# Kernel optimization log

Measured on AMD Instinct MI355X. Metric: run time of the kernel, lower is better.

Reference implementation:

```python
import jax, jax.numpy as jnp
import numpy as np

B, S, H, NH = 32, 512, 2048, 8
HD = H // NH
MAXPOS = 1000


def _sinusoidal_pe():
    pos = np.arange(MAXPOS)[:, None].astype(np.float32)
    div = np.exp(np.arange(0, H, 2).astype(np.float32) * (-np.log(10000.0) / H))
    pe = np.zeros((1, MAXPOS, H), np.float32)
    pe[0, :, 0::2] = np.sin(pos * div)
    pe[0, :, 1::2] = np.cos(pos * div)
    return jnp.asarray(pe)


def setup_inputs() -> dict:
    key = jax.random.key(0)
    ks = jax.random.split(key, 12)
    w = lambda k, shape: jax.random.normal(k, shape, jnp.float32) * 0.02
    return {
        'embeddings': jax.random.normal(ks[0], (B, S, H), jnp.float32),
        'temporal_indices': jax.random.randint(ks[1], (B, S), 0, MAXPOS),
        'pe': _sinusoidal_pe(),
        'in_proj_w': w(ks[2], (3 * H, H)), 'in_proj_b': jnp.zeros((3 * H,), jnp.float32),
        'out_proj_w': w(ks[3], (H, H)), 'out_proj_b': jnp.zeros((H,), jnp.float32),
        'ln1_g': jnp.ones((H,), jnp.float32), 'ln1_b': jnp.zeros((H,), jnp.float32),
        'ffn_w1': w(ks[4], (4 * H, H)), 'ffn_b1': jnp.zeros((4 * H,), jnp.float32),
        'ffn_w2': w(ks[5], (H, 4 * H)), 'ffn_b2': jnp.zeros((H,), jnp.float32),
        'ln2_g': jnp.ones((H,), jnp.float32), 'ln2_b': jnp.zeros((H,), jnp.float32),
        'te_w1': w(ks[6], (H, H)), 'te_b1': jnp.zeros((H,), jnp.float32),
        'te_w2': w(ks[7], (H, H)), 'te_b2': jnp.zeros((H,), jnp.float32),
        'pr_w1': w(ks[8], (H, H)), 'pr_b1': jnp.zeros((H,), jnp.float32),
        'pr_w2': w(ks[9], (H, H)), 'pr_b2': jnp.zeros((H,), jnp.float32),
    }


def _ln(x, g, b, eps=1e-5):
    m = jnp.mean(x, -1, keepdims=True)
    v = jnp.mean((x - m) ** 2, -1, keepdims=True)
    return (x - m) * jax.lax.rsqrt(v + eps) * g + b


def _forward(embeddings, pe, in_proj_w, in_proj_b, out_proj_w, out_proj_b,
             ln1_g, ln1_b, ffn_w1, ffn_b1, ffn_w2, ffn_b2, ln2_g, ln2_b,
             te_w1, te_b1, te_w2, te_b2, pr_w1, pr_b1, pr_w2, pr_b2,
             temporal_indices):
    b, s, h = embeddings.shape
    # temporal positional encoding gather: [B,S,H]
    x = embeddings + pe[0][temporal_indices]
    # packed qkv projection (torch MultiheadAttention in_proj)
    qkv = x @ in_proj_w.T + in_proj_b
    q, k, v = jnp.split(qkv, 3, axis=-1)
    heads = lambda t: t.reshape(b, s, NH, HD).transpose(0, 2, 1, 3)
    q, k, v = heads(q), heads(k), heads(v)
    scores = jnp.einsum('bhqd,bhkd->bhqk', q, k) / jnp.sqrt(jnp.float32(HD))
    a = jax.nn.softmax(scores, axis=-1)
    o = jnp.einsum('bhqk,bhkd->bhqd', a, v).transpose(0, 2, 1, 3).reshape(b, s, h)
    attn = o @ out_proj_w.T + out_proj_b
    # residual + LN, GELU FFN, residual + LN
    h1 = _ln(embeddings + attn, ln1_g, ln1_b)
    f = jax.nn.gelu(h1 @ ffn_w1.T + ffn_b1, approximate=False) @ ffn_w2.T + ffn_b2
    h2 = _ln(h1 + f, ln2_g, ln2_b)
    # temporal_encoder MLP (temporal_info=None branch)
    te = jax.nn.relu(h2 @ te_w1.T + te_b1) @ te_w2.T + te_b2
    # projection head (training-mode path)
    pr = jax.nn.relu(te @ pr_w1.T + pr_b1) @ pr_w2.T + pr_b2
    return pr / jnp.maximum(jnp.linalg.norm(pr, axis=-1, keepdims=True), 1e-12)


def reference(embeddings, temporal_indices, pe, in_proj_w, in_proj_b, out_proj_w,
              out_proj_b, ln1_g, ln1_b, ffn_w1, ffn_b1, ffn_w2, ffn_b2, ln2_g,
              ln2_b, te_w1, te_b1, te_w2, te_b2, pr_w1, pr_b1, pr_w2, pr_b2):
    return _forward(embeddings, pe, in_proj_w, in_proj_b, out_proj_w, out_proj_b,
                    ln1_g, ln1_b, ffn_w1, ffn_b1, ffn_w2, ffn_b2, ln2_g, ln2_b,
                    te_w1, te_b1, te_w2, te_b2, pr_w1, pr_b1, pr_w2, pr_b2,
                    temporal_indices)
```

## Files before the change

### kernel.cpp

```cpp
#include <hip/hip_runtime.h>
#include <math.h>


typedef __bf16 bf16;
typedef __bf16 bf16x8 __attribute__((ext_vector_type(8)));
typedef float f32x4 __attribute__((ext_vector_type(4)));

#define Hdim 2048

#define GLOAD_LDS16(gp, lp)                                          \
  __builtin_amdgcn_global_load_lds(                                  \
      (const __attribute__((address_space(1))) void*)(gp),           \
      (__attribute__((address_space(3))) void*)(lp), 16, 0, 0)

template <int RF>
__global__ __launch_bounds__(256)
void gemm_bt(const bf16* __restrict__ A, int lda, long sA1, long sA2, int zdA,
             const bf16* __restrict__ W, int ldw, long sW1, long sW2, int zdW,
             bf16* __restrict__ C, int ldc, long sC1, long sC2, int zdC,
             const float* __restrict__ bias,
             const void* __restrict__ resp, int ldr,
             int K, float scale, int act)
{
  __shared__ bf16 As[2][128 * 64];
  __shared__ bf16 Ws[2][128 * 64];
  const int tid = threadIdx.x;
  const int z = blockIdx.z;
  A += (size_t)(z / zdA) * sA1 + (size_t)(z % zdA) * sA2;
  W += (size_t)(z / zdW) * sW1 + (size_t)(z % zdW) * sW2;
  C += (size_t)(z / zdC) * sC1 + (size_t)(z % zdC) * sC2;

  const int nwg = gridDim.x * gridDim.y;
  int bid = blockIdx.y * gridDim.x + blockIdx.x;
  bid = (bid & 7) * (nwg >> 3) + (bid >> 3);
  const int m0 = (bid / gridDim.x) * 128, n0 = (bid % gridDim.x) * 128;

  const int sm = tid >> 3;
  const int swz = ((tid & 7) ^ (sm & 7)) * 8;
  const int lane = tid & 63, quad = lane >> 4, lr = lane & 15;
  const int wid = tid >> 6, wm = wid >> 1, wn = wid & 1;
  const int rx = lr & 7;
  const int so0 = ((quad      ) ^ rx) * 8;
  const int so1 = ((quad | 4) ^ rx) * 8;

  f32x4 acc[4][4] = {};

  const bf16* Ag = A + (size_t)(m0 + sm) * lda + swz;
  const bf16* Wg = W + (size_t)(n0 + sm) * ldw + swz;

  const int nt = K >> 6;
#pragma unroll
  for (int s = 0; s < 4; ++s) {
    GLOAD_LDS16(Ag + (size_t)(s * 32) * lda, &As[0][s * 2048 + tid * 8]);
    GLOAD_LDS16(Wg + (size_t)(s * 32) * ldw, &Ws[0][s * 2048 + tid * 8]);
  }
  __syncthreads();

  for (int t = 0; t < nt; ++t) {
    const int cur = t & 1;
    if (t + 1 < nt) {
      const int k0 = (t + 1) << 6;
#pragma unroll
      for (int s = 0; s < 4; ++s) {
        GLOAD_LDS16(Ag + (size_t)(s * 32) * lda + k0, &As[cur ^ 1][s * 2048 + tid * 8]);
        GLOAD_LDS16(Wg + (size_t)(s * 32) * ldw + k0, &Ws[cur ^ 1][s * 2048 + tid * 8]);
      }
    }
    const bf16* Ab = As[cur];
    const bf16* Wb = Ws[cur];
#pragma unroll
    for (int kk = 0; kk < 2; ++kk) {
      const int so = kk ? so1 : so0;
      bf16x8 af[4], bfr[4];
#pragma unroll
      for (int i = 0; i < 4; ++i)
        af[i] = *(const bf16x8*)&Ab[(wm * 64 + i * 16 + lr) * 64 + so];
#pragma unroll
      for (int j = 0; j < 4; ++j)
        bfr[j] = *(const bf16x8*)&Wb[(wn * 64 + j * 16 + lr) * 64 + so];
#pragma unroll
      for (int i = 0; i < 4; ++i)
#pragma unroll
        for (int j = 0; j < 4; ++j)
          acc[i][j] = __builtin_amdgcn_mfma_f32_16x16x32_bf16(af[i], bfr[j], acc[i][j], 0, 0, 0);
    }
    __syncthreads();
  }

  float bj[4];
#pragma unroll
  for (int j = 0; j < 4; ++j)
    bj[j] = bias ? bias[n0 + wn * 64 + j * 16 + lr] : 0.0f;

#pragma unroll
  for (int i = 0; i < 4; ++i) {
#pragma unroll
    for (int r = 0; r < 4; ++r) {
      const int m = m0 + wm * 64 + i * 16 + quad * 4 + r;
#pragma unroll
      for (int j = 0; j < 4; ++j) {
        const int n = n0 + wn * 64 + j * 16 + lr;
        float v = acc[i][j][r] * scale + bj[j];
        if (resp) {
          if (RF) v += ((const float*)resp)[(size_t)m * ldr + n];
          else    v += (float)((const bf16*)resp)[(size_t)m * ldr + n];
        }
        if (act == 1) v = fmaxf(v, 0.0f);
        else if (act == 2) v = 0.5f * v * (1.0f + erff(v * 0.70710678118654752f));
        C[(size_t)m * ldc + n] = (bf16)v;
      }
    }
  }
}

__global__ __launch_bounds__(256)
void cvt_w(const float* __restrict__ src, bf16* __restrict__ dst)
{
  const size_t i = ((size_t)blockIdx.x * 256 + threadIdx.x) * 8;
  float4 a = *(const float4*)&src[i];
  float4 b = *(const float4*)&src[i + 4];
  bf16x8 o;
  o[0] = (bf16)a.x; o[1] = (bf16)a.y; o[2] = (bf16)a.z; o[3] = (bf16)a.w;
  o[4] = (bf16)b.x; o[5] = (bf16)b.y; o[6] = (bf16)b.z; o[7] = (bf16)b.w;
  *(bf16x8*)&dst[i] = o;
}

__global__ __launch_bounds__(256)
void gather_pe(const float* __restrict__ emb, const int* __restrict__ idx,
               const float* __restrict__ pe, bf16* __restrict__ X)
{
  const int m = blockIdx.x;
  const int p = idx[m];
  const size_t off = (size_t)m * Hdim + threadIdx.x * 8;
  const size_t poff = (size_t)p * Hdim + threadIdx.x * 8;
  float4 e0 = *(const float4*)&emb[off];
  float4 e1 = *(const float4*)&emb[off + 4];
  float4 q0 = *(const float4*)&pe[poff];
  float4 q1 = *(const float4*)&pe[poff + 4];
  bf16x8 o;
  o[0] = (bf16)(e0.x + q0.x); o[1] = (bf16)(e0.y + q0.y);
  o[2] = (bf16)(e0.z + q0.z); o[3] = (bf16)(e0.w + q0.w);
  o[4] = (bf16)(e1.x + q1.x); o[5] = (bf16)(e1.y + q1.y);
  o[6] = (bf16)(e1.z + q1.z); o[7] = (bf16)(e1.w + q1.w);
  *(bf16x8*)&X[off] = o;
}

__global__ __launch_bounds__(256)
void softmax_rows(bf16* __restrict__ P)
{
  const int lane = threadIdx.x & 63;
  const size_t row = (size_t)blockIdx.x * 4 + (threadIdx.x >> 6);
  bf16* p = P + row * 512 + lane * 8;
  bf16x8 v = *(const bf16x8*)p;
  float x[8], mx = -1e30f;
#pragma unroll
  for (int j = 0; j < 8; ++j) { x[j] = (float)v[j]; mx = fmaxf(mx, x[j]); }
#pragma unroll
  for (int o = 32; o; o >>= 1) mx = fmaxf(mx, __shfl_xor(mx, o));
  float s = 0.0f;
#pragma unroll
  for (int j = 0; j < 8; ++j) { x[j] = expf(x[j] - mx); s += x[j]; }
#pragma unroll
  for (int o = 32; o; o >>= 1) s += __shfl_xor(s, o);
  const float inv = 1.0f / s;
  bf16x8 ov;
#pragma unroll
  for (int j = 0; j < 8; ++j) ov[j] = (bf16)(x[j] * inv);
  *(bf16x8*)p = ov;
}

__global__ __launch_bounds__(256)
void transpose_v(const bf16* __restrict__ qkv, bf16* __restrict__ vt)
{
  const int z = blockIdx.z, b = z >> 3, h = z & 7;
  const unsigned short* V =
      (const unsigned short*)qkv + (size_t)b * 512 * 6144 + 4096 + h * 256;
  unsigned short* out = (unsigned short*)vt + (size_t)z * 256 * 512;
  const int d0 = blockIdx.x * 64, k0 = blockIdx.y * 64;
  __shared__ unsigned short t[64 * 65];
  const int r = threadIdx.x >> 3;
  const int c8 = (threadIdx.x & 7) * 8;
#pragma unroll
  for (int pass = 0; pass < 2; ++pass) {
    const int rr = r + pass * 32;
    uint4 u = *(const uint4*)(V + (size_t)(k0 + rr) * 6144 + d0 + c8);
    const unsigned short* ep = (const unsigned short*)&u;
#pragma unroll
    for (int j = 0; j < 8; ++j) t[(c8 + j) * 65 + rr] = ep[j];
  }
  __syncthreads();
#pragma unroll
  for (int pass = 0; pass < 2; ++pass) {
    const int dr = r + pass * 32;
    unsigned short e[8];
#pragma unroll
    for (int j = 0; j < 8; ++j) e[j] = t[dr * 65 + c8 + j];
    *(uint4*)(out + (size_t)(d0 + dr) * 512 + k0 + c8) = *(const uint4*)e;
  }
}

__global__ __launch_bounds__(256)
void ln_rows(const bf16* __restrict__ src, const float* __restrict__ g,
             const float* __restrict__ b, bf16* __restrict__ dst)
{
  const size_t off = (size_t)blockIdx.x * Hdim + threadIdx.x * 8;
  bf16x8 v = *(const bf16x8*)&src[off];
  float x[8], s = 0.0f, ss = 0.0f;
#pragma unroll
  for (int j = 0; j < 8; ++j) { x[j] = (float)v[j]; s += x[j]; ss += x[j] * x[j]; }
  __shared__ float red[8];
#pragma unroll
  for (int o = 32; o; o >>= 1) { s += __shfl_xor(s, o); ss += __shfl_xor(ss, o); }
  const int w = threadIdx.x >> 6;
  if ((threadIdx.x & 63) == 0) { red[w] = s; red[4 + w] = ss; }
  __syncthreads();
  s = red[0] + red[1] + red[2] + red[3];
  ss = red[4] + red[5] + red[6] + red[7];
  const float mean = s * (1.0f / Hdim);
  const float var = ss * (1.0f / Hdim) - mean * mean;
  const float rstd = rsqrtf(var + 1e-5f);
  float4 g0 = *(const float4*)&g[threadIdx.x * 8];
  float4 g1 = *(const float4*)&g[threadIdx.x * 8 + 4];
  float4 b0 = *(const float4*)&b[threadIdx.x * 8];
  float4 b1 = *(const float4*)&b[threadIdx.x * 8 + 4];
  const float gg[8] = {g0.x, g0.y, g0.z, g0.w, g1.x, g1.y, g1.z, g1.w};
  const float bb[8] = {b0.x, b0.y, b0.z, b0.w, b1.x, b1.y, b1.z, b1.w};
  bf16x8 ov;
#pragma unroll
  for (int j = 0; j < 8; ++j)
    ov[j] = (bf16)(((x[j] - mean) * rstd) * gg[j] + bb[j]);
  *(bf16x8*)&dst[off] = ov;
}

__global__ __launch_bounds__(256)
void l2norm_rows(const bf16* __restrict__ src, float* __restrict__ dst)
{
  const size_t off = (size_t)blockIdx.x * Hdim + threadIdx.x * 8;
  bf16x8 v = *(const bf16x8*)&src[off];
  float x[8], ss = 0.0f;
#pragma unroll
  for (int j = 0; j < 8; ++j) { x[j] = (float)v[j]; ss += x[j] * x[j]; }
  __shared__ float red[4];
#pragma unroll
  for (int o = 32; o; o >>= 1) ss += __shfl_xor(ss, o);
  const int w = threadIdx.x >> 6;
  if ((threadIdx.x & 63) == 0) red[w] = ss;
  __syncthreads();
  ss = red[0] + red[1] + red[2] + red[3];
  const float inv = 1.0f / fmaxf(sqrtf(ss), 1e-12f);
  float4 o0, o1;
  o0.x = x[0] * inv; o0.y = x[1] * inv; o0.z = x[2] * inv; o0.w = x[3] * inv;
  o1.x = x[4] * inv; o1.y = x[5] * inv; o1.z = x[6] * inv; o1.w = x[7] * inv;
  *(float4*)&dst[off] = o0;
  *(float4*)&dst[off + 4] = o1;
}

extern "C" void kernel_launch(void* const* d_in, const int* in_sizes, int n_in,
                              void* d_out, int out_size, void* d_ws, size_t ws_size,
                              hipStream_t stream)
{
  const float* emb  = (const float*)d_in[0];
  const int*   tix  = (const int*)d_in[1];
  const float* pe   = (const float*)d_in[2];
  const float* Wqkv = (const float*)d_in[3];
  const float* Bqkv = (const float*)d_in[4];
  const float* Wout = (const float*)d_in[5];
  const float* Bout = (const float*)d_in[6];
  const float* ln1g = (const float*)d_in[7];
  const float* ln1b = (const float*)d_in[8];
  const float* Wff1 = (const float*)d_in[9];
  const float* Bff1 = (const float*)d_in[10];
  const float* Wff2 = (const float*)d_in[11];
  const float* Bff2 = (const float*)d_in[12];
  const float* ln2g = (const float*)d_in[13];
  const float* ln2b = (const float*)d_in[14];
  const float* Wte1 = (const float*)d_in[15];
  const float* Bte1 = (const float*)d_in[16];
  const float* Wte2 = (const float*)d_in[17];
  const float* Bte2 = (const float*)d_in[18];
  const float* Wpr1 = (const float*)d_in[19];
  const float* Bpr1 = (const float*)d_in[20];
  const float* Wpr2 = (const float*)d_in[21];
  const float* Bpr2 = (const float*)d_in[22];
  float* OUT = (float*)d_out;

  char* w = (char*)d_ws;
  bf16* RA   = (bf16*)(w);
  bf16* RB   = (bf16*)(w + (64u << 20));
  bf16* QKVc = RB;
  char* ob   = (char*)d_out;
  bf16* Pc   = (bf16*)(ob);
  bf16* VTc  = (bf16*)(ob + (32u << 20));
  bf16* R1   = (bf16*)(ob);
  bf16* F1c  = (bf16*)(ob);
  bf16* WqkvB = (bf16*)(ob + (48u << 20));
  bf16* WoutB = (bf16*)(ob + (72u << 20));
  bf16* Wff1B = (bf16*)(ob + (64u << 20));
  bf16* Wff2B = (bf16*)(ob + (96u << 20));
  bf16* WteB1 = (bf16*)(ob);
  bf16* WteB2 = (bf16*)(ob + (8u << 20));
  bf16* WprB1 = (bf16*)(ob + (16u << 20));
  bf16* WprB2 = (bf16*)(ob + (24u << 20));

  cvt_w<<<6144, 256, 0, stream>>>(Wqkv, WqkvB);
  cvt_w<<<2048, 256, 0, stream>>>(Wout, WoutB);

  gather_pe<<<16384, 256, 0, stream>>>(emb, tix, pe, RA);

  for (int c = 0; c < 4; ++c) {
    const bf16* Xc = RA + (size_t)c * 4096 * 2048;
    bf16* Oc = RA + (size_t)c * 4096 * 2048;

    gemm_bt<0><<<dim3(48, 32, 1), 256, 0, stream>>>(
        Xc, 2048, 0, 0, 1, WqkvB, 2048, 0, 0, 1, QKVc, 6144, 0, 0, 1,
        Bqkv, nullptr, 0, 2048, 1.0f, 0);

    gemm_bt<0><<<dim3(4, 4, 64), 256, 0, stream>>>(
        QKVc, 6144, 3145728L, 256, 8,
        QKVc + 2048, 6144, 3145728L, 256, 8,
        Pc, 512, 262144L, 0, 1,
        nullptr, nullptr, 0, 256, 0.0625f, 0);

    softmax_rows<<<8192, 256, 0, stream>>>(Pc);

    transpose_v<<<dim3(4, 8, 64), 256, 0, stream>>>(QKVc, VTc);

    gemm_bt<0><<<dim3(2, 4, 64), 256, 0, stream>>>(
        Pc, 512, 262144L, 0, 1,
        VTc, 512, 131072L, 0, 1,
        Oc, 2048, 1048576L, 256, 8,
        nullptr, nullptr, 0, 512, 1.0f, 0);
  }

  gemm_bt<1><<<dim3(16, 128, 1), 256, 0, stream>>>(
      RA, 2048, 0, 0, 1, WoutB, 2048, 0, 0, 1, R1, 2048, 0, 0, 1,
      Bout, emb, 2048, 2048, 1.0f, 0);

  cvt_w<<<8192, 256, 0, stream>>>(Wff1, Wff1B);
  cvt_w<<<8192, 256, 0, stream>>>(Wff2, Wff2B);

  ln_rows<<<16384, 256, 0, stream>>>(R1, ln1g, ln1b, RA);

  for (int f = 0; f < 8; ++f) {
    const bf16* H1f = RA + (size_t)f * 2048 * 2048;
    bf16* R2f = RB + (size_t)f * 2048 * 2048;
    gemm_bt<0><<<dim3(64, 16, 1), 256, 0, stream>>>(
        H1f, 2048, 0, 0, 1, Wff1B, 2048, 0, 0, 1, F1c, 8192, 0, 0, 1,
        Bff1, nullptr, 0, 2048, 1.0f, 2);
    gemm_bt<0><<<dim3(16, 16, 1), 256, 0, stream>>>(
        F1c, 8192, 0, 0, 1, Wff2B, 8192, 0, 0, 1, R2f, 2048, 0, 0, 1,
        Bff2, H1f, 2048, 8192, 1.0f, 0);
  }

  cvt_w<<<2048, 256, 0, stream>>>(Wte1, WteB1);
  cvt_w<<<2048, 256, 0, stream>>>(Wte2, WteB2);
  cvt_w<<<2048, 256, 0, stream>>>(Wpr1, WprB1);
  cvt_w<<<2048, 256, 0, stream>>>(Wpr2, WprB2);

  ln_rows<<<16384, 256, 0, stream>>>(RB, ln2g, ln2b, RA);

  gemm_bt<0><<<dim3(16, 128, 1), 256, 0, stream>>>(
      RA, 2048, 0, 0, 1, WteB1, 2048, 0, 0, 1, RB, 2048, 0, 0, 1,
      Bte1, nullptr, 0, 2048, 1.0f, 1);

  gemm_bt<0><<<dim3(16, 128, 1), 256, 0, stream>>>(
      RB, 2048, 0, 0, 1, WteB2, 2048, 0, 0, 1, RA, 2048, 0, 0, 1,
      Bte2, nullptr, 0, 2048, 1.0f, 0);

  gemm_bt<0><<<dim3(16, 128, 1), 256, 0, stream>>>(
      RA, 2048, 0, 0, 1, WprB1, 2048, 0, 0, 1, RB, 2048, 0, 0, 1,
      Bpr1, nullptr, 0, 2048, 1.0f, 1);

  gemm_bt<0><<<dim3(16, 128, 1), 256, 0, stream>>>(
      RB, 2048, 0, 0, 1, WprB2, 2048, 0, 0, 1, RA, 2048, 0, 0, 1,
      Bpr2, nullptr, 0, 2048, 1.0f, 0);

  l2norm_rows<<<16384, 256, 0, stream>>>(RA, OUT);
}
```

Before: 4.113 ms.

## Add 256x256-tile 8-wave GEMM with interleaved LDS staging for dense projections

Introduces a new 512-thread GEMM kernel using 256x256 output tiles, double-buffered LDS split into halves, and a phased schedule that interleaves global-to-LDS loads with MFMA work, using barriers and setprio. All large dense projections (QKV, out-proj, FFN, temporal and projection MLPs) switch to it. The FFN loop now uses 4096-row chunks instead of 2048. The larger tiles raise arithmetic intensity and overlap loads with compute, at the cost of high register and LDS use (128 KB LDS) and fewer workgroups per launch.

```diff
diff --git a/kernel.cpp b/kernel.cpp
--- a/kernel.cpp
+++ b/kernel.cpp
@@ -12,6 +12,139 @@
   __builtin_amdgcn_global_load_lds(                                  \
       (const __attribute__((address_space(1))) void*)(gp),           \
       (__attribute__((address_space(3))) void*)(lp), 16, 0, 0)
+
+
+#define STG(X, OP, H)                                                         \
+  {                                                                           \
+    const int _buf = (X) & 1;                                                 \
+    const bf16* _g = (OP) ? Wg : Ag;                                          \
+    const long _ld = (OP) ? ldw : lda;                                        \
+    const long _ro = (long)((H) * 128) * _ld + (long)(X) * 64;                \
+    bf16* _d = &L[(((_buf * 2 + (OP)) * 2 + (H)) * 8192) + tid * 8];          \
+    GLOAD_LDS16(_g + _ro, _d);                                                \
+    GLOAD_LDS16(_g + _ro + 64 * _ld, _d + 4096);                              \
+  }
+
+#define PH(SLOT, Q, STAGES, GATE)                                             \
+  {                                                                           \
+    if ((Q) == 0) {                                                           \
+      _Pragma("unroll")                                                       \
+      for (int nj = 0; nj < 4; ++nj) {                                        \
+        const int rb = offB[SLOT] + (rbB + nj * 16 + lr) * 64;                \
+        bq[nj][0] = *(const bf16x8*)&L[rb + so0];                             \
+        bq[nj][1] = *(const bf16x8*)&L[rb + so1];                             \
+      }                                                                       \
+    }                                                                         \
+    bf16x8 a00, a01, a10, a11;                                                \
+    {                                                                         \
+      const int r0 = offA[SLOT] + ((Q) * 32 + lr) * 64;                       \
+      a00 = *(const bf16x8*)&L[r0 + so0];                                     \
+      a01 = *(const bf16x8*)&L[r0 + so1];                                     \
+      a10 = *(const bf16x8*)&L[r0 + 1024 + so0];                              \
+      a11 = *(const bf16x8*)&L[r0 + 1024 + so1];                              \
+    }                                                                         \
+    STAGES;                                                                   \
+    GATE;                                                                     \
+    __builtin_amdgcn_s_barrier();                                             \
+    asm volatile("s_waitcnt lgkmcnt(0)" ::: "memory");                        \
+    __builtin_amdgcn_sched_barrier(0);                                        \
+    __builtin_amdgcn_s_setprio(1);                                            \
+    _Pragma("unroll")                                                         \
+    for (int nj = 0; nj < 4; ++nj) {                                          \
+      acc[(Q)*2][nj]   = __builtin_amdgcn_mfma_f32_16x16x32_bf16(a00, bq[nj][0], acc[(Q)*2][nj], 0, 0, 0);   \
+      acc[(Q)*2+1][nj] = __builtin_amdgcn_mfma_f32_16x16x32_bf16(a10, bq[nj][0], acc[(Q)*2+1][nj], 0, 0, 0); \
+    }                                                                         \
+    _Pragma("unroll")                                                         \
+    for (int nj = 0; nj < 4; ++nj) {                                          \
+      acc[(Q)*2][nj]   = __builtin_amdgcn_mfma_f32_16x16x32_bf16(a01, bq[nj][1], acc[(Q)*2][nj], 0, 0, 0);   \
+      acc[(Q)*2+1][nj] = __builtin_amdgcn_mfma_f32_16x16x32_bf16(a11, bq[nj][1], acc[(Q)*2+1][nj], 0, 0, 0); \
+    }                                                                         \
+    __builtin_amdgcn_s_setprio(0);                                            \
+    __builtin_amdgcn_sched_barrier(0);                                        \
+    __builtin_amdgcn_s_barrier();                                             \
+  }
+
+template <int RF>
+__global__ __launch_bounds__(512, 2)
+void gemm256(const bf16* __restrict__ A, int lda,
+             const bf16* __restrict__ W, int ldw,
+             bf16* __restrict__ C, int ldc,
+             const float* __restrict__ bias,
+             const void* __restrict__ resp, int ldr,
+             int K, float scale, int act)
+{
+  __shared__ bf16 L[8 * 8192];
+  const int tid = threadIdx.x;
+
+  const int nwg = gridDim.x * gridDim.y;
+  int bid = blockIdx.y * gridDim.x + blockIdx.x;
+  bid = (bid & 7) * (nwg >> 3) + (bid >> 3);
+  const int m0 = (bid / gridDim.x) * 256, n0 = (bid % gridDim.x) * 256;
+
+  const int lane = tid & 63, quad = lane >> 4, lr = lane & 15;
+  const int wid = tid >> 6, wm = wid >> 2, wn = wid & 3;
+  const int rx = lr & 7;
+  const int so0 = (quad ^ rx) * 8;
+  const int so1 = so0 ^ 32;
+  const int rbB = (wn & 1) * 64;
+  const int offA[2] = { wm * 8192, (4 + wm) * 8192 };
+  const int offB[2] = { (2 + (wn >> 1)) * 8192, (6 + (wn >> 1)) * 8192 };
+
+  const int srow = tid >> 3;
+  const int scol = ((tid & 7) ^ (srow & 7)) * 8;
+  const bf16* Ag = A + (size_t)(m0 + srow) * lda + scol;
+  const bf16* Wg = W + (size_t)(n0 + srow) * ldw + scol;
+
+  f32x4 acc[8][4] = {};
+  bf16x8 bq[4][2];
+
+  const int nt = K >> 6;
+
+  STG(0, 1, 0); STG(0, 1, 1); STG(0, 0, 0); STG(0, 0, 1);
+  STG(1, 1, 0); STG(1, 1, 1);
+  asm volatile("s_waitcnt vmcnt(4)" ::: "memory");
+  __builtin_amdgcn_s_barrier();
+
+  for (int t0 = 0; t0 < nt; t0 += 2) {
+    const int nl = (t0 + 2 < nt);
+    PH(0, 0, STG(t0 + 1, 0, 0), );
+    PH(0, 1, STG(t0 + 1, 0, 1), );
+    PH(0, 2, if (nl) STG(t0 + 2, 1, 0), );
+    PH(0, 3, if (nl) STG(t0 + 2, 1, 1),
+             if (nl) { asm volatile("s_waitcnt vmcnt(4)" ::: "memory"); }
+             else    { asm volatile("s_waitcnt vmcnt(0)" ::: "memory"); });
+    PH(1, 0, if (nl) STG(t0 + 2, 0, 0), );
+    PH(1, 1, if (nl) STG(t0 + 2, 0, 1), );
+    PH(1, 2, if (nl) STG(t0 + 3, 1, 0), );
+    PH(1, 3, if (nl) STG(t0 + 3, 1, 1),
+             if (nl) { asm volatile("s_waitcnt vmcnt(4)" ::: "memory"); });
+  }
+
+  float bj[4];
+#pragma unroll
+  for (int nj = 0; nj < 4; ++nj)
+    bj[nj] = bias ? bias[n0 + wn * 64 + nj * 16 + lr] : 0.0f;
+
+#pragma unroll
+  for (int mi = 0; mi < 8; ++mi) {
+#pragma unroll
+    for (int rr = 0; rr < 4; ++rr) {
+      const int m = m0 + wm * 128 + mi * 16 + quad * 4 + rr;
+#pragma unroll
+      for (int nj = 0; nj < 4; ++nj) {
+        const int n = n0 + wn * 64 + nj * 16 + lr;
+        float v = acc[mi][nj][rr] * scale + bj[nj];
+        if (resp) {
+          if (RF) v += ((const float*)resp)[(size_t)m * ldr + n];
+          else    v += (float)((const bf16*)resp)[(size_t)m * ldr + n];
+        }
+        if (act == 1) v = fmaxf(v, 0.0f);
+        else if (act == 2) v = 0.5f * v * (1.0f + erff(v * 0.70710678118654752f));
+        C[(size_t)m * ldc + n] = (bf16)v;
+      }
+    }
+  }
+}
 
 template <int RF>
 __global__ __launch_bounds__(256)
@@ -40,7 +173,7 @@
   const int lane = tid & 63, quad = lane >> 4, lr = lane & 15;
   const int wid = tid >> 6, wm = wid >> 1, wn = wid & 1;
   const int rx = lr & 7;
-  const int so0 = ((quad      ) ^ rx) * 8;
+  const int so0 = ((quad) ^ rx) * 8;
   const int so1 = ((quad | 4) ^ rx) * 8;
 
   f32x4 acc[4][4] = {};
@@ -311,9 +444,8 @@
     const bf16* Xc = RA + (size_t)c * 4096 * 2048;
     bf16* Oc = RA + (size_t)c * 4096 * 2048;
 
-    gemm_bt<0><<<dim3(48, 32, 1), 256, 0, stream>>>(
-        Xc, 2048, 0, 0, 1, WqkvB, 2048, 0, 0, 1, QKVc, 6144, 0, 0, 1,
-        Bqkv, nullptr, 0, 2048, 1.0f, 0);
+    gemm256<0><<<dim3(24, 16), 512, 0, stream>>>(
+        Xc, 2048, WqkvB, 2048, QKVc, 6144, Bqkv, nullptr, 0, 2048, 1.0f, 0);
 
     gemm_bt<0><<<dim3(4, 4, 64), 256, 0, stream>>>(
         QKVc, 6144, 3145728L, 256, 8,
@@ -332,24 +464,21 @@
         nullptr, nullptr, 0, 512, 1.0f, 0);
   }
 
-  gemm_bt<1><<<dim3(16, 128, 1), 256, 0, stream>>>(
-      RA, 2048, 0, 0, 1, WoutB, 2048, 0, 0, 1, R1, 2048, 0, 0, 1,
-      Bout, emb, 2048, 2048, 1.0f, 0);
+  gemm256<1><<<dim3(8, 64), 512, 0, stream>>>(
+      RA, 2048, WoutB, 2048, R1, 2048, Bout, emb, 2048, 2048, 1.0f, 0);
 
   cvt_w<<<8192, 256, 0, stream>>>(Wff1, Wff1B);
   cvt_w<<<8192, 256, 0, stream>>>(Wff2, Wff2B);
 
   ln_rows<<<16384, 256, 0, stream>>>(R1, ln1g, ln1b, RA);
 
-  for (int f = 0; f < 8; ++f) {
-    const bf16* H1f = RA + (size_t)f * 2048 * 2048;
-    bf16* R2f = RB + (size_t)f * 2048 * 2048;
-    gemm_bt<0><<<dim3(64, 16, 1), 256, 0, stream>>>(
-        H1f, 2048, 0, 0, 1, Wff1B, 2048, 0, 0, 1, F1c, 8192, 0, 0, 1,
-        Bff1, nullptr, 0, 2048, 1.0f, 2);
-    gemm_bt<0><<<dim3(16, 16, 1), 256, 0, stream>>>(
-        F1c, 8192, 0, 0, 1, Wff2B, 8192, 0, 0, 1, R2f, 2048, 0, 0, 1,
-        Bff2, H1f, 2048, 8192, 1.0f, 0);
+  for (int f = 0; f < 4; ++f) {
+    const bf16* H1f = RA + (size_t)f * 4096 * 2048;
+    bf16* R2f = RB + (size_t)f * 4096 * 2048;
+    gemm256<0><<<dim3(32, 16), 512, 0, stream>>>(
+        H1f, 2048, Wff1B, 2048, F1c, 8192, Bff1, nullptr, 0, 2048, 1.0f, 2);
+    gemm256<0><<<dim3(8, 16), 512, 0, stream>>>(
+        F1c, 8192, Wff2B, 8192, R2f, 2048, Bff2, H1f, 2048, 8192, 1.0f, 0);
   }
 
   cvt_w<<<2048, 256, 0, stream>>>(Wte1, WteB1);
@@ -359,21 +488,17 @@
 
   ln_rows<<<16384, 256, 0, stream>>>(RB, ln2g, ln2b, RA);
 
-  gemm_bt<0><<<dim3(16, 128, 1), 256, 0, stream>>>(
-      RA, 2048, 0, 0, 1, WteB1, 2048, 0, 0, 1, RB, 2048, 0, 0, 1,
-      Bte1, nullptr, 0, 2048, 1.0f, 1);
-
-  gemm_bt<0><<<dim3(16, 128, 1), 256, 0, stream>>>(
-      RB, 2048, 0, 0, 1, WteB2, 2048, 0, 0, 1, RA, 2048, 0, 0, 1,
-      Bte2, nullptr, 0, 2048, 1.0f, 0);
-
-  gemm_bt<0><<<dim3(16, 128, 1), 256, 0, stream>>>(
-      RA, 2048, 0, 0, 1, WprB1, 2048, 0, 0, 1, RB, 2048, 0, 0, 1,
-      Bpr1, nullptr, 0, 2048, 1.0f, 1);
-
-  gemm_bt<0><<<dim3(16, 128, 1), 256, 0, stream>>>(
-      RB, 2048, 0, 0, 1, WprB2, 2048, 0, 0, 1, RA, 2048, 0, 0, 1,
-      Bpr2, nullptr, 0, 2048, 1.0f, 0);
+  gemm256<0><<<dim3(8, 64), 512, 0, stream>>>(
+      RA, 2048, WteB1, 2048, RB, 2048, Bte1, nullptr, 0, 2048, 1.0f, 1);
+
+  gemm256<0><<<dim3(8, 64), 512, 0, stream>>>(
+      RB, 2048, WteB2, 2048, RA, 2048, Bte2, nullptr, 0, 2048, 1.0f, 0);
+
+  gemm256<0><<<dim3(8, 64), 512, 0, stream>>>(
+      RA, 2048, WprB1, 2048, RB, 2048, Bpr1, nullptr, 0, 2048, 1.0f, 1);
+
+  gemm256<0><<<dim3(8, 64), 512, 0, stream>>>(
+      RB, 2048, WprB2, 2048, RA, 2048, Bpr2, nullptr, 0, 2048, 1.0f, 0);
 
   l2norm_rows<<<16384, 256, 0, stream>>>(RA, OUT);
 }
```

After: 3.518 ms. 1.17x faster.
